# Performance work log

Hardware: AMD Instinct MI355X
Metric: run time of the kernel (lower is better)

The kernel has to match this reference:

```python
import jax, jax.numpy as jnp
import numpy as np
import math

N_HEAD = 16
N_KV_HEAD = 4
HEAD_DIM = 128  # n_embed // n_head


def apply_rope(x, omega, offset=0):
    # x: (B, T, H, D); omega: (D//2,) Llama-style inverse frequencies
    T = x.shape[1]
    d2 = x.shape[-1] // 2
    pos = (jnp.arange(T) + offset).astype(x.dtype)
    ang = pos[:, None] * omega[None, :]              # (T, d2)
    cos = jnp.cos(ang)[None, :, None, :]
    sin = jnp.sin(ang)[None, :, None, :]
    x1, x2 = x[..., :d2], x[..., d2:]
    return jnp.concatenate([x1 * cos - x2 * sin, x1 * sin + x2 * cos], axis=-1)


def setup_inputs() -> dict:
    key = jax.random.key(0)
    k1, k2, k3, k4 = jax.random.split(key, 4)
    B, T, C = 2, 2048, 2048
    std = 0.02
    x = jax.random.normal(k1, (B, T, C), dtype=jnp.float32)
    wq = jax.random.normal(k2, (C, C), dtype=jnp.float32) * std
    wkv = jax.random.normal(k3, (C, 2 * N_KV_HEAD * HEAD_DIM), dtype=jnp.float32) * std
    wproj = jax.random.normal(k4, (C, C), dtype=jnp.float32) * std * (2 * 24) ** (-0.5)
    # Llama RoPE frequencies: 1 / 10000^(2i/D)
    omega = (1.0 / (10000.0 ** (jnp.arange(0, HEAD_DIM, 2, dtype=jnp.float32) / HEAD_DIM)))
    return {"x": x, "wq": wq, "wkv": wkv, "wproj": wproj, "omega": omega}


def reference(x, wq, wkv, wproj, omega):
    B, T, C = x.shape
    H, KH, D = N_HEAD, N_KV_HEAD, HEAD_DIM
    G = H // KH  # query heads per kv head

    q = (x @ wq).reshape(B, T, H, D)
    kv = x @ wkv
    k, v = jnp.split(kv, 2, axis=-1)

    q = apply_rope(q, omega, offset=0)
    k = apply_rope(k.reshape(B, T, KH, D), omega, offset=0)
    v = v.reshape(B, T, KH, D)

    # GQA causal attention (no KV expansion: group query heads per kv head)
    qr = q.reshape(B, T, KH, G, D)
    scores = jnp.einsum('bqkgd,bskd->bkgqs', qr, k) / math.sqrt(D)
    causal = jnp.tril(jnp.ones((T, T), dtype=bool))
    scores = jnp.where(causal[None, None, None, :, :], scores, -jnp.inf)
    att = jax.nn.softmax(scores, axis=-1)
    y = jnp.einsum('bkgqs,bskd->bqkgd', att, v).reshape(B, T, C)
    return y @ wproj
```

## Files before the change

### kernel.cpp

```cpp
#include <hip/hip_runtime.h>
#include <hip/hip_bf16.h>

#define B_ 2
#define T_ 2048
#define C_ 2048
#define H_ 16
#define KH_ 4
#define D_ 128

typedef unsigned short ushort_t;
typedef __attribute__((ext_vector_type(8))) short short8;
typedef __attribute__((ext_vector_type(4))) float f32x4;

#define RSQRT_D 0.08838834764831845f
#define L2E 1.4426950408889634f
#define QSCALE (0.08838834764831845f * 1.4426950408889634f)

__device__ __forceinline__ ushort_t f2b(float f) {
  union { float f; unsigned u; } v; v.f = f;
  unsigned r = v.u + 0x7fffu + ((v.u >> 16) & 1u);
  return (ushort_t)(r >> 16);
}
__device__ __forceinline__ float b2f(ushort_t u) {
  union { unsigned u; float f; } v; v.u = ((unsigned)u) << 16;
  return v.f;
}

__device__ __forceinline__ f32x4 mfma16(short8 a, short8 b, f32x4 c) {
  return __builtin_amdgcn_mfma_f32_16x16x32_bf16(a, b, c, 0, 0, 0);
}

__device__ __forceinline__ void async16(const void* g, void* l) {
  __builtin_amdgcn_global_load_lds(
      (const __attribute__((address_space(1))) void*)g,
      (__attribute__((address_space(3))) void*)l, 16, 0, 0);
}

__device__ __forceinline__ unsigned cvtpk(float lo, float hi) {
  unsigned r;
  asm volatile("v_cvt_pk_bf16_f32 %0, %1, %2" : "=v"(r) : "v"(lo), "v"(hi));
  return r;
}


__global__ void convert_f32_bf16(const float* __restrict__ in, ushort_t* __restrict__ out, int n4) {
  int i = blockIdx.x * blockDim.x + threadIdx.x;
  if (i >= n4) return;
  float4 v = ((const float4*)in)[i];
  ushort4 o;
  o.x = f2b(v.x); o.y = f2b(v.y); o.z = f2b(v.z); o.w = f2b(v.w);
  ((ushort4*)out)[i] = o;
}

__global__ void transpose_to_bf16(const float* __restrict__ in, ushort_t* __restrict__ out, int R, int C) {
  __shared__ float tile[32][33];
  int c0 = blockIdx.x * 32, r0 = blockIdx.y * 32;
  int tx = threadIdx.x, ty = threadIdx.y;
#pragma unroll
  for (int i = 0; i < 4; i++) {
    int r = ty + i * 8;
    tile[r][tx] = in[(size_t)(r0 + r) * C + c0 + tx];
  }
  __syncthreads();
#pragma unroll
  for (int i = 0; i < 4; i++) {
    int r = ty + i * 8;
    out[(size_t)(c0 + r) * R + r0 + tx] = f2b(tile[tx][r]);
  }
}

__global__ void rope_tab_k(const float* __restrict__ omega, float2* __restrict__ tab) {
  int idx = blockIdx.x * blockDim.x + threadIdx.x;
  int d = idx & 63;
  int t = idx >> 6;
  float ang = (float)t * omega[d];
  tab[idx] = make_float2(cosf(ang), sinf(ang));
}

__global__ void rope_q_k(const ushort_t* __restrict__ QKVraw, const float2* __restrict__ tab,
                         ushort_t* __restrict__ Qb) {
  int idx = blockIdx.x * blockDim.x + threadIdx.x;
  int d = idx & 63;
  int h = (idx >> 6) & 15;
  int t = (idx >> 10) & 2047;
  int b = idx >> 21;
  size_t in_off = (size_t)(b * 2048 + t) * 3072 + h * 128 + d;
  float x1 = b2f(QKVraw[in_off]);
  float x2 = b2f(QKVraw[in_off + 64]);
  float2 cs = tab[t * 64 + d];
  size_t out_off = ((size_t)(b * 16 + h) * 2048 + t) * 128 + d;
  Qb[out_off] = f2b((x1 * cs.x - x2 * cs.y) * QSCALE);
  Qb[out_off + 64] = f2b((x1 * cs.y + x2 * cs.x) * QSCALE);
}

__global__ void rope_k_k(const ushort_t* __restrict__ QKVraw, const float2* __restrict__ tab,
                         ushort_t* __restrict__ Kb) {
  int idx = blockIdx.x * blockDim.x + threadIdx.x;
  int d = idx & 63;
  int kh = (idx >> 6) & 3;
  int t = (idx >> 8) & 2047;
  int b = idx >> 19;
  size_t in_off = (size_t)(b * 2048 + t) * 3072 + 2048 + kh * 128 + d;
  float x1 = b2f(QKVraw[in_off]);
  float x2 = b2f(QKVraw[in_off + 64]);
  float2 cs = tab[t * 64 + d];
  size_t out_off = ((size_t)(b * 4 + kh) * 2048 + t) * 128 + d;
  Kb[out_off] = f2b(x1 * cs.x - x2 * cs.y);
  Kb[out_off + 64] = f2b(x1 * cs.y + x2 * cs.x);
}

__global__ void v_frag_k(const ushort_t* __restrict__ QKVraw, ushort_t* __restrict__ Vf) {
  int idx = blockIdx.x * blockDim.x + threadIdx.x;
  int lane = idx & 63;
  int n = (idx >> 6) & 7;
  int hv = (idx >> 9) & 1;
  int tile = (idx >> 10) & 31;
  int z = idx >> 15;
  int b = z >> 2, kh = z & 3;
  int lr = lane & 15, lc = lane >> 4;
  int d = n * 16 + lr;
  union { ushort_t u[8]; short8 v; } out;
#pragma unroll
  for (int j = 0; j < 8; j++) {
    int tw = j >> 1, par = j & 1;
    int kl = (hv * 2 + (tw >> 1)) * 16 + lc * 4 + 2 * (tw & 1) + par;
    int t = tile * 64 + kl;
    out.u[j] = QKVraw[(size_t)(b * 2048 + t) * 3072 + 2560 + kh * 128 + d];
  }
  *(short8*)(Vf + (size_t)idx * 8) = out.v;
}


__device__ __forceinline__ void store_out(float* C, size_t idx, float v) { C[idx] = v; }
__device__ __forceinline__ void store_out(ushort_t* C, size_t idx, float v) { C[idx] = f2b(v); }

template <typename OUT_T>
__global__ __launch_bounds__(256) void gemm_bt(const ushort_t* __restrict__ A,
                                               const ushort_t* __restrict__ Bt,
                                               OUT_T* __restrict__ C,
                                               int M, int N, int K) {
  __shared__ __attribute__((aligned(16))) ushort_t As[2][128 * 32];
  __shared__ __attribute__((aligned(16))) ushort_t Bs[2][128 * 32];
  const int tid = threadIdx.x;
  const int lane = tid & 63;
  const int w = tid >> 6;
  const int bm = blockIdx.y, bn = blockIdx.x;
  const int lr = lane & 15, lc = lane >> 4;
  const int wr = (w >> 1) * 64, wc = (w & 1) * 64;
  const ushort_t* Ab = A + (size_t)bm * 128 * K;
  const ushort_t* Bb = Bt + (size_t)bn * 128 * K;
  const int srow = tid >> 2;
  const int scol = (tid & 3) * 8;
  f32x4 acc[4][4];
#pragma unroll
  for (int i = 0; i < 4; i++)
#pragma unroll
    for (int j = 0; j < 4; j++) acc[i][j] = (f32x4)(0.0f);

  async16(Ab + (size_t)srow * K + scol, &As[0][0] + srow * 32 + scol);
  async16(Ab + (size_t)(srow + 64) * K + scol, &As[0][0] + (srow + 64) * 32 + scol);
  async16(Bb + (size_t)srow * K + scol, &Bs[0][0] + srow * 32 + scol);
  async16(Bb + (size_t)(srow + 64) * K + scol, &Bs[0][0] + (srow + 64) * 32 + scol);

  const int nt = K >> 5;
#pragma unroll 2
  for (int t = 0; t < nt - 1; t++) {
    const int cur = t & 1;
    {
      const int k1 = (t + 1) << 5;
      ushort_t* Ad = &As[cur ^ 1][0];
      ushort_t* Bd = &Bs[cur ^ 1][0];
      async16(Ab + (size_t)srow * K + k1 + scol, Ad + srow * 32 + scol);
      async16(Ab + (size_t)(srow + 64) * K + k1 + scol, Ad + (srow + 64) * 32 + scol);
      async16(Bb + (size_t)srow * K + k1 + scol, Bd + srow * 32 + scol);
      async16(Bb + (size_t)(srow + 64) * K + k1 + scol, Bd + (srow + 64) * 32 + scol);
    }
    asm volatile("s_waitcnt vmcnt(4)" ::: "memory");
    __builtin_amdgcn_s_barrier();
    __builtin_amdgcn_sched_barrier(0);
    const ushort_t* Al = &As[cur][0];
    const ushort_t* Bl = &Bs[cur][0];
    short8 af[4], bf[4];
#pragma unroll
    for (int mi = 0; mi < 4; mi++)
      af[mi] = *(const short8*)(Al + (wr + mi * 16 + lr) * 32 + lc * 8);
#pragma unroll
    for (int ni = 0; ni < 4; ni++)
      bf[ni] = *(const short8*)(Bl + (wc + ni * 16 + lr) * 32 + lc * 8);
#pragma unroll
    for (int mi = 0; mi < 4; mi++)
#pragma unroll
      for (int ni = 0; ni < 4; ni++)
        acc[mi][ni] = mfma16(af[mi], bf[ni], acc[mi][ni]);
    asm volatile("" ::: "memory");
    __builtin_amdgcn_s_barrier();
    asm volatile("" ::: "memory");
  }
  {
    const int cur = (nt - 1) & 1;
    asm volatile("s_waitcnt vmcnt(0)" ::: "memory");
    __builtin_amdgcn_s_barrier();
    __builtin_amdgcn_sched_barrier(0);
    const ushort_t* Al = &As[cur][0];
    const ushort_t* Bl = &Bs[cur][0];
    short8 af[4], bf[4];
#pragma unroll
    for (int mi = 0; mi < 4; mi++)
      af[mi] = *(const short8*)(Al + (wr + mi * 16 + lr) * 32 + lc * 8);
#pragma unroll
    for (int ni = 0; ni < 4; ni++)
      bf[ni] = *(const short8*)(Bl + (wc + ni * 16 + lr) * 32 + lc * 8);
#pragma unroll
    for (int mi = 0; mi < 4; mi++)
#pragma unroll
      for (int ni = 0; ni < 4; ni++)
        acc[mi][ni] = mfma16(af[mi], bf[ni], acc[mi][ni]);
  }
#pragma unroll
  for (int mi = 0; mi < 4; mi++) {
#pragma unroll
    for (int ni = 0; ni < 4; ni++) {
      int row = bm * 128 + wr + mi * 16 + lc * 4;
      int col = bn * 128 + wc + ni * 16 + lr;
#pragma unroll
      for (int r = 0; r < 4; r++)
        store_out(C, (size_t)(row + r) * N + col, acc[mi][ni][r]);
    }
  }
}

__global__ __launch_bounds__(256, 2) void attn_k(const ushort_t* __restrict__ Qb,
                                                 const ushort_t* __restrict__ Kb,
                                                 const ushort_t* __restrict__ Vf,
                                                 ushort_t* __restrict__ Yb) {
  __shared__ __attribute__((aligned(16))) ushort_t Ks[2][64 * 128];
  const int tid = threadIdx.x;
  const int lane = tid & 63;
  const int w = tid >> 6;
  const int lr = lane & 15, lc = lane >> 4;
  const int gy = blockIdx.y;
  const int h = gy;
  const int b = blockIdx.z;
  const int kh = h >> 2;
  const int qc = b ? (15 - ((blockIdx.x + gy) & 15)) : ((blockIdx.x + gy) & 15);
  const int q0w = qc * 128 + w * 32;

  const ushort_t* Qp = Qb + (size_t)(b * 16 + h) * T_ * D_;
  const ushort_t* Kp = Kb + (size_t)(b * 4 + kh) * T_ * D_;
  const ushort_t* Vfb = Vf + (size_t)(b * 4 + kh) * 262144;

  const int st_row = tid >> 4;
  const int st_slot = tid & 15;

  short8 qf[2][4];
#pragma unroll
  for (int f = 0; f < 2; f++)
#pragma unroll
    for (int c = 0; c < 4; c++)
      qf[f][c] = *(const short8*)(Qp + (size_t)(q0w + f * 16 + lr) * D_ + c * 32 + lc * 8);

  f32x4 o[2][8];
#pragma unroll
  for (int f = 0; f < 2; f++)
#pragma unroll
    for (int n = 0; n < 8; n++) o[f][n] = (f32x4)(0.0f);
  float m[2] = {-1e30f, -1e30f}, l[2] = {0.0f, 0.0f};

  const int nt = 2 * qc + 2;

#pragma unroll
  for (int i = 0; i < 4; i++) {
    int row = i * 16 + st_row;
    async16(Kp + (size_t)row * D_ + (((st_slot - row) & 15) * 8),
            &Ks[0][0] + row * 128 + st_slot * 8);
  }

#pragma unroll 1
  for (int ti = 0; ti < nt; ti++) {
    __syncthreads();
    const int kv0 = ti * 64;
    if (ti + 1 < nt) {
      const ushort_t* Kn = Kp + (size_t)(kv0 + 64) * D_;
      ushort_t* dst = &Ks[(ti + 1) & 1][0];
#pragma unroll
      for (int i = 0; i < 4; i++) {
        int row = i * 16 + st_row;
        async16(Kn + (size_t)row * D_ + (((st_slot - row) & 15) * 8),
                dst + row * 128 + st_slot * 8);
      }
    }
    if (kv0 > q0w + 31) continue;
    const ushort_t* Kl = &Ks[ti & 1][0];
    const ushort_t* Vt0 = Vfb + (size_t)(ti * 2) * 4096;
    short8 vr0[8];
#pragma unroll
    for (int n = 0; n < 8; n++)
      vr0[n] = *(const short8*)(Vt0 + n * 512 + lane * 8);
    f32x4 s[2][4];
#pragma unroll
    for (int f = 0; f < 2; f++)
#pragma unroll
      for (int kj = 0; kj < 4; kj++) s[f][kj] = (f32x4)(0.0f);
    __builtin_amdgcn_s_setprio(1);
#pragma unroll
    for (int c = 0; c < 4; c++) {
      short8 kf[4];
#pragma unroll
      for (int kj = 0; kj < 4; kj++)
        kf[kj] = *(const short8*)(Kl + (kj * 16 + lr) * 128 + (((c * 4 + lc + lr) & 15) * 8));
#pragma unroll
      for (int f = 0; f < 2; f++)
#pragma unroll
        for (int kj = 0; kj < 4; kj++)
          s[f][kj] = mfma16(kf[kj], qf[f][c], s[f][kj]);
    }
    __builtin_amdgcn_s_setprio(0);
    const ushort_t* Vt1 = Vfb + (size_t)(ti * 2 + 1) * 4096;
    short8 vr1[8];
#pragma unroll
    for (int n = 0; n < 8; n++)
      vr1[n] = *(const short8*)(Vt1 + n * 512 + lane * 8);
    const bool maskt = (kv0 + 63 > q0w);
    union { unsigned u[4]; short8 v; } pa0[2], pa1[2];
#pragma unroll
    for (int f = 0; f < 2; f++) {
      const int q = q0w + f * 16 + lr;
      float pv[16];
      float mx = -1e30f;
      if (maskt) {
#pragma unroll
        for (int kj = 0; kj < 4; kj++)
#pragma unroll
          for (int r = 0; r < 4; r++) {
            float a = s[f][kj][r];
            if (kv0 + kj * 16 + lc * 4 + r > q) a = -1e30f;
            pv[kj * 4 + r] = a;
            mx = fmaxf(mx, a);
          }
      } else {
#pragma unroll
        for (int kj = 0; kj < 4; kj++)
#pragma unroll
          for (int r = 0; r < 4; r++) {
            float a = s[f][kj][r];
            pv[kj * 4 + r] = a;
            mx = fmaxf(mx, a);
          }
      }
      mx = fmaxf(mx, __shfl_xor(mx, 16));
      mx = fmaxf(mx, __shfl_xor(mx, 32));
      const bool need = __any(mx > m[f] + 8.0f);
      const float mn = need ? fmaxf(m[f], mx) : m[f];
      float rs = 0.0f;
#pragma unroll
      for (int i = 0; i < 16; i++) {
        pv[i] = exp2f(pv[i] - mn);
        rs += pv[i];
      }
      rs += __shfl_xor(rs, 16);
      rs += __shfl_xor(rs, 32);
#pragma unroll
      for (int kj = 0; kj < 2; kj++) {
        pa0[f].u[kj * 2] = cvtpk(pv[kj * 4], pv[kj * 4 + 1]);
        pa0[f].u[kj * 2 + 1] = cvtpk(pv[kj * 4 + 2], pv[kj * 4 + 3]);
        pa1[f].u[kj * 2] = cvtpk(pv[8 + kj * 4], pv[8 + kj * 4 + 1]);
        pa1[f].u[kj * 2 + 1] = cvtpk(pv[8 + kj * 4 + 2], pv[8 + kj * 4 + 3]);
      }
      if (need) {
        float al = exp2f(m[f] - mn);
        m[f] = mn;
        l[f] = l[f] * al + rs;
        float alT[4];
#pragma unroll
        for (int r = 0; r < 4; r++)
          alT[r] = __shfl(al, (lane & 48) | (lc * 4 + r));
#pragma unroll
        for (int n = 0; n < 8; n++)
#pragma unroll
          for (int r = 0; r < 4; r++) o[f][n][r] *= alT[r];
      } else {
        l[f] += rs;
      }
    }
    __builtin_amdgcn_s_setprio(1);
#pragma unroll
    for (int n = 0; n < 8; n++) {
      o[0][n] = mfma16(pa0[0].v, vr0[n], o[0][n]);
      o[1][n] = mfma16(pa0[1].v, vr0[n], o[1][n]);
    }
#pragma unroll
    for (int n = 0; n < 8; n++) {
      o[0][n] = mfma16(pa1[0].v, vr1[n], o[0][n]);
      o[1][n] = mfma16(pa1[1].v, vr1[n], o[1][n]);
    }
    __builtin_amdgcn_s_setprio(0);
  }
#pragma unroll
  for (int f = 0; f < 2; f++) {
    float inv = 1.0f / l[f];
    float invT[4];
#pragma unroll
    for (int r = 0; r < 4; r++)
      invT[r] = __shfl(inv, (lane & 48) | (lc * 4 + r));
#pragma unroll
    for (int n = 0; n < 8; n++)
#pragma unroll
      for (int r = 0; r < 4; r++) {
        int qo = q0w + f * 16 + lc * 4 + r;
        int d = n * 16 + lr;
        Yb[(size_t)(b * T_ + qo) * 2048 + h * 128 + d] = f2b(o[f][n][r] * invT[r]);
      }
  }
}


extern "C" void kernel_launch(void* const* d_in, const int* in_sizes, int n_in,
                              void* d_out, int out_size, void* d_ws, size_t ws_size,
                              hipStream_t stream) {
  (void)in_sizes; (void)n_in; (void)out_size; (void)ws_size;
  const float* x = (const float*)d_in[0];
  const float* wq = (const float*)d_in[1];
  const float* wkv = (const float*)d_in[2];
  const float* wproj = (const float*)d_in[3];
  const float* omega = (const float*)d_in[4];
  float* out = (float*)d_out;
  char* ws = (char*)d_ws;

  ushort_t* xb     = (ushort_t*)(ws + 0);
  ushort_t* wqkvT  = (ushort_t*)(ws + 16777216);
  ushort_t* wkvT   = (ushort_t*)(ws + 25165824);
  ushort_t* wprojT = (ushort_t*)(ws + 29360128);
  ushort_t* QKVraw = (ushort_t*)(ws + 37748736);
  ushort_t* Qb     = (ushort_t*)(ws + 62914560);
  ushort_t* Kb     = (ushort_t*)(ws + 79691776);
  ushort_t* Vf     = (ushort_t*)(ws + 83886080);
  ushort_t* Yb     = (ushort_t*)(ws + 88080384);
  float2*   tab    = (float2*)(ws + 104857600);

  convert_f32_bf16<<<8192, 256, 0, stream>>>(x, xb, 2097152);
  transpose_to_bf16<<<dim3(64, 64), dim3(32, 8), 0, stream>>>(wq, wqkvT, 2048, 2048);
  transpose_to_bf16<<<dim3(32, 64), dim3(32, 8), 0, stream>>>(wkv, wkvT, 2048, 1024);
  transpose_to_bf16<<<dim3(64, 64), dim3(32, 8), 0, stream>>>(wproj, wprojT, 2048, 2048);
  rope_tab_k<<<512, 256, 0, stream>>>(omega, tab);

  gemm_bt<<<dim3(24, 32), 256, 0, stream>>>(xb, wqkvT, QKVraw, 4096, 3072, 2048);

  rope_q_k<<<16384, 256, 0, stream>>>(QKVraw, tab, Qb);
  rope_k_k<<<4096, 256, 0, stream>>>(QKVraw, tab, Kb);
  v_frag_k<<<1024, 256, 0, stream>>>(QKVraw, Vf);

  attn_k<<<dim3(16, 16, 2), 256, 0, stream>>>(Qb, Kb, Vf, Yb);

  gemm_bt<<<dim3(16, 32), 256, 0, stream>>>(Yb, wprojT, out, 4096, 2048, 2048);
}
```

Baseline: 221.0 us.

## Split long causal query blocks across two workgroups and merge partial softmax results

The attention kernel now processes 24 work items per head instead of 16. Query blocks 8-15 have their KV range split into two halves, each handled by its own workgroup that writes unnormalized partial outputs and row max/sum statistics to workspace. A new merge kernel combines each pair with log-sum-exp weighting and writes the final bf16 output. The goal is to balance work across blocks and cut the causal tail, at the cost of an extra launch, extra global traffic, and rounding the partial outputs to bf16.

Result: slower. 241.6 us (+9.3%).

```diff
diff --git a/kernel.cpp b/kernel.cpp
--- a/kernel.cpp
+++ b/kernel.cpp
@@ -229,21 +229,29 @@
   }
 }
 
+static __device__ const signed char c_s[24] = {15,15,7,14,14,13,13,6,12,12,11,11,5,10,10,9,9,4,8,8,3,2,1,0};
+static __device__ const signed char c_h[24] = {0,1,-1,0,1,0,1,-1,0,1,0,1,-1,0,1,0,1,-1,0,1,-1,-1,-1,-1};
+
 __global__ __launch_bounds__(256, 2) void attn_k(const ushort_t* __restrict__ Qb,
                                                  const ushort_t* __restrict__ Kb,
                                                  const ushort_t* __restrict__ Vf,
-                                                 ushort_t* __restrict__ Yb) {
+                                                 ushort_t* __restrict__ Yb,
+                                                 ushort_t* __restrict__ Po,
+                                                 float* __restrict__ Pstat) {
   __shared__ __attribute__((aligned(16))) ushort_t Ks[2][64 * 128];
   const int tid = threadIdx.x;
   const int lane = tid & 63;
   const int w = tid >> 6;
   const int lr = lane & 15, lc = lane >> 4;
-  const int gy = blockIdx.y;
-  const int h = gy;
+  const int h = blockIdx.y;
   const int b = blockIdx.z;
   const int kh = h >> 2;
-  const int qc = b ? (15 - ((blockIdx.x + gy) & 15)) : ((blockIdx.x + gy) & 15);
-  const int q0w = qc * 128 + w * 32;
+  const int item = blockIdx.x;
+  const int s = c_s[item];
+  const int hf = c_h[item];
+  const int t0 = (hf == 1) ? (s + 1) : 0;
+  const int t1 = (hf == 0) ? (s + 1) : (2 * s + 2);
+  const int q0w = s * 128 + w * 32;
 
   const ushort_t* Qp = Qb + (size_t)(b * 16 + h) * T_ * D_;
   const ushort_t* Kp = Kb + (size_t)(b * 4 + kh) * T_ * D_;
@@ -266,20 +274,18 @@
     for (int n = 0; n < 8; n++) o[f][n] = (f32x4)(0.0f);
   float m[2] = {-1e30f, -1e30f}, l[2] = {0.0f, 0.0f};
 
-  const int nt = 2 * qc + 2;
-
 #pragma unroll
   for (int i = 0; i < 4; i++) {
     int row = i * 16 + st_row;
-    async16(Kp + (size_t)row * D_ + (((st_slot - row) & 15) * 8),
-            &Ks[0][0] + row * 128 + st_slot * 8);
+    async16(Kp + (size_t)(t0 * 64 + row) * D_ + (((st_slot - row) & 15) * 8),
+            &Ks[t0 & 1][0] + row * 128 + st_slot * 8);
   }
 
 #pragma unroll 1
-  for (int ti = 0; ti < nt; ti++) {
+  for (int ti = t0; ti < t1; ti++) {
     __syncthreads();
     const int kv0 = ti * 64;
-    if (ti + 1 < nt) {
+    if (ti + 1 < t1) {
       const ushort_t* Kn = Kp + (size_t)(kv0 + 64) * D_;
       ushort_t* dst = &Ks[(ti + 1) & 1][0];
 #pragma unroll
@@ -296,11 +302,11 @@
 #pragma unroll
     for (int n = 0; n < 8; n++)
       vr0[n] = *(const short8*)(Vt0 + n * 512 + lane * 8);
-    f32x4 s[2][4];
+    f32x4 s_[2][4];
 #pragma unroll
     for (int f = 0; f < 2; f++)
 #pragma unroll
-      for (int kj = 0; kj < 4; kj++) s[f][kj] = (f32x4)(0.0f);
+      for (int kj = 0; kj < 4; kj++) s_[f][kj] = (f32x4)(0.0f);
     __builtin_amdgcn_s_setprio(1);
 #pragma unroll
     for (int c = 0; c < 4; c++) {
@@ -312,7 +318,7 @@
       for (int f = 0; f < 2; f++)
 #pragma unroll
         for (int kj = 0; kj < 4; kj++)
-          s[f][kj] = mfma16(kf[kj], qf[f][c], s[f][kj]);
+          s_[f][kj] = mfma16(kf[kj], qf[f][c], s_[f][kj]);
     }
     __builtin_amdgcn_s_setprio(0);
     const ushort_t* Vt1 = Vfb + (size_t)(ti * 2 + 1) * 4096;
@@ -332,7 +338,7 @@
         for (int kj = 0; kj < 4; kj++)
 #pragma unroll
           for (int r = 0; r < 4; r++) {
-            float a = s[f][kj][r];
+            float a = s_[f][kj][r];
             if (kv0 + kj * 16 + lc * 4 + r > q) a = -1e30f;
             pv[kj * 4 + r] = a;
             mx = fmaxf(mx, a);
@@ -342,7 +348,7 @@
         for (int kj = 0; kj < 4; kj++)
 #pragma unroll
           for (int r = 0; r < 4; r++) {
-            float a = s[f][kj][r];
+            float a = s_[f][kj][r];
             pv[kj * 4 + r] = a;
             mx = fmaxf(mx, a);
           }
@@ -395,21 +401,72 @@
     }
     __builtin_amdgcn_s_setprio(0);
   }
-#pragma unroll
-  for (int f = 0; f < 2; f++) {
-    float inv = 1.0f / l[f];
-    float invT[4];
-#pragma unroll
-    for (int r = 0; r < 4; r++)
-      invT[r] = __shfl(inv, (lane & 48) | (lc * 4 + r));
-#pragma unroll
-    for (int n = 0; n < 8; n++)
-#pragma unroll
-      for (int r = 0; r < 4; r++) {
-        int qo = q0w + f * 16 + lc * 4 + r;
-        int d = n * 16 + lr;
-        Yb[(size_t)(b * T_ + qo) * 2048 + h * 128 + d] = f2b(o[f][n][r] * invT[r]);
+
+  if (hf < 0) {
+#pragma unroll
+    for (int f = 0; f < 2; f++) {
+      float inv = 1.0f / l[f];
+      float invT[4];
+#pragma unroll
+      for (int r = 0; r < 4; r++)
+        invT[r] = __shfl(inv, (lane & 48) | (lc * 4 + r));
+#pragma unroll
+      for (int n = 0; n < 8; n++)
+#pragma unroll
+        for (int r = 0; r < 4; r++) {
+          int qo = q0w + f * 16 + lc * 4 + r;
+          int d = n * 16 + lr;
+          Yb[(size_t)(b * T_ + qo) * 2048 + h * 128 + d] = f2b(o[f][n][r] * invT[r]);
+        }
+    }
+  } else {
+    const int pidx = ((b * 16 + h) * 8 + (s - 8)) * 2 + hf;
+    ushort_t* Op = Po + (size_t)pidx * 16384;
+    float* St = Pstat + (size_t)pidx * 256;
+#pragma unroll
+    for (int f = 0; f < 2; f++) {
+#pragma unroll
+      for (int n = 0; n < 8; n++)
+#pragma unroll
+        for (int r = 0; r < 4; r++) {
+          int ql = w * 32 + f * 16 + lc * 4 + r;
+          Op[ql * 128 + n * 16 + lr] = f2b(o[f][n][r]);
+        }
+      if (lc == 0) {
+        St[w * 32 + f * 16 + lr] = m[f];
+        St[128 + w * 32 + f * 16 + lr] = l[f];
       }
+    }
+  }
+}
+
+__global__ void merge_k(const ushort_t* __restrict__ Po, const float* __restrict__ Pstat,
+                        ushort_t* __restrict__ Yb) {
+  const int inst = blockIdx.x;
+  const int si = inst & 7;
+  const int h = (inst >> 3) & 15;
+  const int b = inst >> 7;
+  const int s = 8 + si;
+  const int p0 = inst * 2, p1 = p0 + 1;
+  const int row = threadIdx.x >> 1;
+  const int c0 = (threadIdx.x & 1) * 64;
+  const float m1 = Pstat[p0 * 256 + row], l1 = Pstat[p0 * 256 + 128 + row];
+  const float m2 = Pstat[p1 * 256 + row], l2 = Pstat[p1 * 256 + 128 + row];
+  const float M = fmaxf(m1, m2);
+  const float w1 = exp2f(m1 - M), w2 = exp2f(m2 - M);
+  const float inv = 1.0f / (l1 * w1 + l2 * w2);
+  const ushort_t* O1 = Po + (size_t)p0 * 16384 + row * 128 + c0;
+  const ushort_t* O2 = Po + (size_t)p1 * 16384 + row * 128 + c0;
+  ushort_t* Y = Yb + (size_t)(b * T_ + s * 128 + row) * 2048 + h * 128 + c0;
+#pragma unroll
+  for (int j8 = 0; j8 < 8; j8++) {
+    union { ushort_t u[8]; short8 v; } a, bb, r;
+    a.v = *(const short8*)(O1 + j8 * 8);
+    bb.v = *(const short8*)(O2 + j8 * 8);
+#pragma unroll
+    for (int e = 0; e < 8; e++)
+      r.u[e] = f2b((b2f(a.u[e]) * w1 + b2f(bb.u[e]) * w2) * inv);
+    *(short8*)(Y + j8 * 8) = r.v;
   }
 }
 
@@ -436,6 +493,8 @@
   ushort_t* Vf     = (ushort_t*)(ws + 83886080);
   ushort_t* Yb     = (ushort_t*)(ws + 88080384);
   float2*   tab    = (float2*)(ws + 104857600);
+  ushort_t* Po     = (ushort_t*)(ws + 0);
+  float*    Pstat  = (float*)(ws + 17825792);
 
   convert_f32_bf16<<<8192, 256, 0, stream>>>(x, xb, 2097152);
   transpose_to_bf16<<<dim3(64, 64), dim3(32, 8), 0, stream>>>(wq, wqkvT, 2048, 2048);
@@ -449,7 +508,8 @@
   rope_k_k<<<4096, 256, 0, stream>>>(QKVraw, tab, Kb);
   v_frag_k<<<1024, 256, 0, stream>>>(QKVraw, Vf);
 
-  attn_k<<<dim3(16, 16, 2), 256, 0, stream>>>(Qb, Kb, Vf, Yb);
+  attn_k<<<dim3(24, 16, 2), 256, 0, stream>>>(Qb, Kb, Vf, Yb, Po, Pstat);
+  merge_k<<<256, 256, 0, stream>>>(Po, Pstat, Yb);
 
   gemm_bt<<<dim3(16, 32), 256, 0, stream>>>(Yb, wprojT, out, 4096, 2048, 2048);
 }
```

## Use 256x256-tile 512-thread GEMM with fine-grained async pipelining for QKV projection

Applied to the files above, without the earlier changes.

Adds a new GEMM kernel that uses 256x256 output tiles, 8 waves and a 64-wide K step split into four 32-wide half-stages. Each stage is loaded with async copies into a swizzled LDS layout and interleaved with MFMA groups. Wave priority is raised around the MFMA work. Only the QKV projection uses it, cutting global/LDS traffic per flop. The trade-off is only 192 blocks on a 256-CU part, leaving some CUs idle, plus higher register pressure from 32 accumulators.

After: 223.1 us. About the same (+0.9%).

```diff
diff --git a/kernel.cpp b/kernel.cpp
--- a/kernel.cpp
+++ b/kernel.cpp
@@ -130,9 +130,9 @@
   *(short8*)(Vf + (size_t)idx * 8) = out.v;
 }
 
-
 __device__ __forceinline__ void store_out(float* C, size_t idx, float v) { C[idx] = v; }
 __device__ __forceinline__ void store_out(ushort_t* C, size_t idx, float v) { C[idx] = f2b(v); }
+
 
 template <typename OUT_T>
 __global__ __launch_bounds__(256) void gemm_bt(const ushort_t* __restrict__ A,
@@ -229,6 +229,154 @@
   }
 }
 
+template <typename OUT_T>
+__global__ __launch_bounds__(512, 1) void gemm256(const ushort_t* __restrict__ A,
+                                                  const ushort_t* __restrict__ Bt,
+                                                  OUT_T* __restrict__ C,
+                                                  int M, int N, int K) {
+  __shared__ __attribute__((aligned(16))) ushort_t As[2][2][8192];
+  __shared__ __attribute__((aligned(16))) ushort_t Bs[2][2][8192];
+  const int tid = threadIdx.x;
+  const int lane = tid & 63;
+  const int w = tid >> 6;
+  const int lr = lane & 15, lc = lane >> 4;
+  const int wm = w >> 2, wn = w & 3;
+  const int bm = blockIdx.y, bn = blockIdx.x;
+  const ushort_t* Ab = A + (size_t)bm * 256 * K;
+  const ushort_t* Bb = Bt + (size_t)bn * 256 * K;
+  const int sr0 = tid >> 2, sc0 = tid & 3;
+  const int sr1 = 128 + (tid >> 2), sc1 = tid & 3;
+
+  f32x4 acc[8][4];
+#pragma unroll
+  for (int i = 0; i < 8; i++)
+#pragma unroll
+    for (int j = 0; j < 4; j++) acc[i][j] = (f32x4)(0.0f);
+
+  auto STAGE = [&](int kt, int hid) {
+    const int buf = kt & 1;
+    const int kk = hid >> 1;
+    const ushort_t* gb = (hid & 1) ? Bb : Ab;
+    ushort_t* db = (hid & 1) ? &Bs[buf][kk][0] : &As[buf][kk][0];
+    const int kbase = kt * 64 + kk * 32;
+    {
+      const int lch = sc0 ^ ((sr0 >> 1) & 3);
+      async16(gb + (size_t)sr0 * K + kbase + lch * 8, db + (sr0 * 4 + sc0) * 8);
+    }
+    {
+      const int lch = sc1 ^ ((sr1 >> 1) & 3);
+      async16(gb + (size_t)sr1 * K + kbase + lch * 8, db + (sr1 * 4 + sc1) * 8);
+    }
+  };
+
+  const int nt = K >> 6;
+  STAGE(0, 0); STAGE(0, 1); STAGE(0, 2); STAGE(0, 3);
+
+#pragma unroll 1
+  for (int t = 0; t < nt; ++t) {
+    const int buf = t & 1;
+    const ushort_t* Ak0 = &As[buf][0][0];
+    const ushort_t* Ak1 = &As[buf][1][0];
+    const ushort_t* Bk0 = &Bs[buf][0][0];
+    const ushort_t* Bk1 = &Bs[buf][1][0];
+    short8 af[4], bf[4];
+
+    if (t + 1 < nt) STAGE(t + 1, 0);
+    asm volatile("s_waitcnt vmcnt(6)" ::: "memory");
+    __builtin_amdgcn_s_barrier();
+    __builtin_amdgcn_sched_barrier(0);
+#pragma unroll
+    for (int nf = 0; nf < 4; nf++) {
+      const int row = wn * 64 + nf * 16 + lr;
+      bf[nf] = *(const short8*)(Bk0 + row * 32 + ((lc ^ ((row >> 1) & 3)) * 8));
+    }
+#pragma unroll
+    for (int mf = 0; mf < 4; mf++) {
+      const int row = wm * 128 + mf * 16 + lr;
+      af[mf] = *(const short8*)(Ak0 + row * 32 + ((lc ^ ((row >> 1) & 3)) * 8));
+    }
+    __builtin_amdgcn_s_setprio(1);
+#pragma unroll
+    for (int mf = 0; mf < 4; mf++)
+#pragma unroll
+      for (int nf = 0; nf < 4; nf++)
+        acc[mf][nf] = mfma16(af[mf], bf[nf], acc[mf][nf]);
+    __builtin_amdgcn_s_setprio(0);
+
+    if (t + 1 < nt) STAGE(t + 1, 1);
+    asm volatile("" ::: "memory");
+    __builtin_amdgcn_s_barrier();
+    __builtin_amdgcn_sched_barrier(0);
+#pragma unroll
+    for (int mf = 0; mf < 4; mf++) {
+      const int row = wm * 128 + 64 + mf * 16 + lr;
+      af[mf] = *(const short8*)(Ak0 + row * 32 + ((lc ^ ((row >> 1) & 3)) * 8));
+    }
+    __builtin_amdgcn_s_setprio(1);
+#pragma unroll
+    for (int mf = 0; mf < 4; mf++)
+#pragma unroll
+      for (int nf = 0; nf < 4; nf++)
+        acc[4 + mf][nf] = mfma16(af[mf], bf[nf], acc[4 + mf][nf]);
+    __builtin_amdgcn_s_setprio(0);
+
+    if (t + 1 < nt) STAGE(t + 1, 2);
+    if (t == nt - 1) {
+      asm volatile("s_waitcnt vmcnt(0)" ::: "memory");
+    } else {
+      asm volatile("s_waitcnt vmcnt(6)" ::: "memory");
+    }
+    __builtin_amdgcn_s_barrier();
+    __builtin_amdgcn_sched_barrier(0);
+#pragma unroll
+    for (int nf = 0; nf < 4; nf++) {
+      const int row = wn * 64 + nf * 16 + lr;
+      bf[nf] = *(const short8*)(Bk1 + row * 32 + ((lc ^ ((row >> 1) & 3)) * 8));
+    }
+#pragma unroll
+    for (int mf = 0; mf < 4; mf++) {
+      const int row = wm * 128 + mf * 16 + lr;
+      af[mf] = *(const short8*)(Ak1 + row * 32 + ((lc ^ ((row >> 1) & 3)) * 8));
+    }
+    __builtin_amdgcn_s_setprio(1);
+#pragma unroll
+    for (int mf = 0; mf < 4; mf++)
+#pragma unroll
+      for (int nf = 0; nf < 4; nf++)
+        acc[mf][nf] = mfma16(af[mf], bf[nf], acc[mf][nf]);
+    __builtin_amdgcn_s_setprio(0);
+
+    if (t + 1 < nt) STAGE(t + 1, 3);
+    asm volatile("" ::: "memory");
+    __builtin_amdgcn_s_barrier();
+    __builtin_amdgcn_sched_barrier(0);
+#pragma unroll
+    for (int mf = 0; mf < 4; mf++) {
+      const int row = wm * 128 + 64 + mf * 16 + lr;
+      af[mf] = *(const short8*)(Ak1 + row * 32 + ((lc ^ ((row >> 1) & 3)) * 8));
+    }
+    __builtin_amdgcn_s_setprio(1);
+#pragma unroll
+    for (int mf = 0; mf < 4; mf++)
+#pragma unroll
+      for (int nf = 0; nf < 4; nf++)
+        acc[4 + mf][nf] = mfma16(af[mf], bf[nf], acc[4 + mf][nf]);
+    __builtin_amdgcn_s_setprio(0);
+  }
+
+#pragma unroll
+  for (int mfp = 0; mfp < 8; mfp++) {
+#pragma unroll
+    for (int nf = 0; nf < 4; nf++) {
+      const int row = bm * 256 + wm * 128 + mfp * 16 + lc * 4;
+      const int col = bn * 256 + wn * 64 + nf * 16 + lr;
+#pragma unroll
+      for (int r = 0; r < 4; r++)
+        store_out(C, (size_t)(row + r) * N + col, acc[mfp][nf][r]);
+    }
+  }
+}
+
 __global__ __launch_bounds__(256, 2) void attn_k(const ushort_t* __restrict__ Qb,
                                                  const ushort_t* __restrict__ Kb,
                                                  const ushort_t* __restrict__ Vf,
@@ -443,7 +591,7 @@
   transpose_to_bf16<<<dim3(64, 64), dim3(32, 8), 0, stream>>>(wproj, wprojT, 2048, 2048);
   rope_tab_k<<<512, 256, 0, stream>>>(omega, tab);
 
-  gemm_bt<<<dim3(24, 32), 256, 0, stream>>>(xb, wqkvT, QKVraw, 4096, 3072, 2048);
+  gemm256<<<dim3(12, 16), 512, 0, stream>>>(xb, wqkvT, QKVraw, 4096, 3072, 2048);
 
   rope_q_k<<<16384, 256, 0, stream>>>(QKVraw, tab, Qb);
   rope_k_k<<<4096, 256, 0, stream>>>(QKVraw, tab, Kb);
```
